# Kernel tuning notes

Measured on AMD Instinct MI355X. Metric: run time of the kernel, lower is better.

The kernel has to match this reference:

```python
import jax, jax.numpy as jnp
import numpy as np
from jax import lax


def _conv3x3(x, w, groups=1):
    # x: [B,C,H,W], w: [O, C//groups, 3, 3], padding=1, no bias
    return lax.conv_general_dilated(
        x, w, window_strides=(1, 1), padding=((1, 1), (1, 1)),
        dimension_numbers=('NCHW', 'OIHW', 'NCHW'),
        feature_group_count=groups)


def _nonlocal_attention(x):
    # q = k = v = flattened features; attn is [B, N, N] with N = H*W
    B, C, H, W = x.shape
    f = x.reshape(B, C, H * W)                                   # [B,C,N]
    attn = jax.nn.softmax(jnp.einsum('bcn,bcm->bnm', f, f), -1)  # [B,N,N]
    out = jnp.einsum('bnm,bcm->bcn', attn, f)                    # [B,C,N]
    return out.reshape(B, C, H, W)


def setup_inputs() -> dict:
    key = jax.random.key(0)
    k1, k2 = jax.random.split(key)
    C = 64
    x = jax.random.normal(k1, (8, C, 64, 64), dtype=jnp.float32)
    # kaiming_normal fan_out for 3x3 conv: std = sqrt(2 / (C*9))
    W_std = jax.random.normal(k2, (C, C, 3, 3), dtype=jnp.float32) * np.float32(np.sqrt(2.0 / (C * 9)))
    return {'x': x, 'W_std': W_std}


def reference(x, W_std):
    B, C, H, W = x.shape
    # FusionDiffConv: standard 3x3 conv + fixed depthwise Laplacian conv
    lap = jnp.array([[0., 1., 0.], [1., -4., 1.], [0., 1., 0.]], dtype=x.dtype)
    W_lap = jnp.broadcast_to(lap[None, None], (C, 1, 3, 3))
    feat = _conv3x3(x, W_std) + _conv3x3(x, W_lap, groups=C)
    # AttentionModule: 3-scale pooled non-local attention pyramid, bilinear upsample, sum
    out = jnp.zeros_like(feat)
    for scale in (4, 2, 1):
        h, w = H // scale, W // scale
        blk = feat.reshape(B, C, h, scale, w, scale).mean(axis=(3, 5))  # adaptive_avg_pool2d (exact divisor)
        blk = _nonlocal_attention(blk)
        # bilinear, half-pixel centers == torch align_corners=False
        out = out + jax.image.resize(blk, (B, C, H, W), method='bilinear')
    return x + out
```

## Files before the change

kernel.cpp:

```cpp
#include <hip/hip_runtime.h>
#include <hip/hip_bf16.h>
#include <math.h>

#define BB 8
#define CC 64
#define HH 64
#define WW 64
#define NPIX (HH*WW)
#define LOG2E 1.44269504088896340736f

typedef __attribute__((ext_vector_type(8))) short bf16x8;
typedef __attribute__((ext_vector_type(8))) _Float16 half8;
typedef __attribute__((ext_vector_type(4))) _Float16 half4;
typedef __attribute__((ext_vector_type(4))) float floatx4;
typedef __attribute__((ext_vector_type(8))) unsigned short ushort8;

__device__ inline unsigned short f2bf(float x) {
  __hip_bfloat16 h = __float2bfloat16(x);
  return *reinterpret_cast<unsigned short*>(&h);
}
__device__ inline unsigned short f2bf_fast(float x) {
  const unsigned u = __float_as_uint(x);
  return (unsigned short)((u + 0x8000u) >> 16);
}
__device__ inline float bf2f(unsigned short u) {
  __hip_bfloat16 h = *reinterpret_cast<__hip_bfloat16*>(&u);
  return __bfloat162float(h);
}
__device__ inline unsigned short f2h(float x) {
  _Float16 h = (_Float16)x;
  return *reinterpret_cast<unsigned short*>(&h);
}
__device__ inline float h2f(unsigned short u) {
  _Float16 h = *reinterpret_cast<_Float16*>(&u);
  return (float)h;
}

__device__ inline int swzoff(int n, int c) {
  return (((c >> 3) ^ (n & 7)) << 3) | (c & 7);
}
__device__ inline int swzvslot(int key, int c) {
  return ((((key >> 2) ^ (c & 15)) << 2)) | (key & 3);
}

#define GLD_LDS16(gp, lp)                                                     \
  __builtin_amdgcn_global_load_lds(                                           \
      (const __attribute__((address_space(1))) void*)(gp),                    \
      (__attribute__((address_space(3))) void*)(lp), 16, 0, 0)

__global__ __launch_bounds__(256) void prep_kernel(
    const float* __restrict__ xin, const float* __restrict__ w,
    unsigned short* __restrict__ xth, unsigned short* __restrict__ xtl,
    unsigned short* __restrict__ wth, unsigned short* __restrict__ wtl) {
  __shared__ float XL[64][65];
  const int bid = blockIdx.x;
  const int tid = threadIdx.x;
  if (bid < 512) {
    const int y = bid & 63, b = bid >> 6;
    const int xq = tid & 15, cw = tid >> 4;
    const float* xb = xin + (size_t)b * CC * NPIX + y * WW;
#pragma unroll
    for (int p = 0; p < 4; ++p) {
      const int c = p * 16 + cw;
      const float4 v = *(const float4*)(xb + (size_t)c * NPIX + xq * 4);
      XL[c][xq * 4 + 0] = v.x; XL[c][xq * 4 + 1] = v.y;
      XL[c][xq * 4 + 2] = v.z; XL[c][xq * 4 + 3] = v.w;
    }
    __syncthreads();
    const int px = tid & 63, cp = tid >> 6;
    const size_t nb = ((size_t)b * NPIX + y * WW + px) * CC;
    ushort8 vh[2], vl[2];
#pragma unroll
    for (int j = 0; j < 16; ++j) {
      const float v = XL[cp * 16 + j][px];
      const unsigned short hh = f2bf(v);
      vh[j >> 3][j & 7] = hh;
      vl[j >> 3][j & 7] = f2bf(v - bf2f(hh));
    }
#pragma unroll
    for (int k = 0; k < 2; ++k) {
      const int ch = cp * 2 + k;
      const int off = ((ch ^ (px & 7)) << 3);
      *(ushort8*)(xth + nb + off) = vh[k];
      *(ushort8*)(xtl + nb + off) = vl[k];
    }
  } else {
    const int idx = (bid - 512) * 256 + tid;
    const int c   = idx & 63;
    const int o   = (idx >> 6) & 63;
    const int tap = idx >> 12;
    float v = w[((o * 64 + c) * 9) + tap];
    if (o == c) {
      const float lapk[9] = {0.f, 1.f, 0.f, 1.f, -4.f, 1.f, 0.f, 1.f, 0.f};
      v += lapk[tap];
    }
    const unsigned short hi = f2bf(v);
    wth[(tap * 64 + o) * 64 + c] = hi;
    wtl[(tap * 64 + o) * 64 + c] = f2bf(v - bf2f(hi));
  }
}

__global__ __launch_bounds__(256, 2) void conv_mfma(
    const unsigned short* __restrict__ xth,
    const unsigned short* __restrict__ xtl,
    const unsigned short* __restrict__ wth,
    const unsigned short* __restrict__ wtl,
    unsigned short* __restrict__ fh, unsigned short* __restrict__ fl,
    unsigned short* __restrict__ fv) {
  __shared__ __align__(16) unsigned short XS[6 * 4096];

  const int tid  = threadIdx.x;
  const int lane = tid & 63;
  const int wave = tid >> 6;
  const int r16  = lane & 15;
  const int quad = lane >> 4;
  const int y = blockIdx.x, b = blockIdx.y;

#pragma unroll
  for (int r = 0; r < 3; ++r) {
    const int yy = min(max(y - 1 + r, 0), HH - 1);
    const unsigned short* sh = xth + ((size_t)b * NPIX + yy * WW) * CC;
    const unsigned short* sl = xtl + ((size_t)b * NPIX + yy * WW) * CC;
    GLD_LDS16(sh + tid * 8,        &XS[r * 4096 + tid * 8]);
    GLD_LDS16(sh + 2048 + tid * 8, &XS[r * 4096 + 2048 + tid * 8]);
    GLD_LDS16(sl + tid * 8,        &XS[(3 + r) * 4096 + tid * 8]);
    GLD_LDS16(sl + 2048 + tid * 8, &XS[(3 + r) * 4096 + 2048 + tid * 8]);
  }
  __syncthreads();

  floatx4 acc[4];
#pragma unroll
  for (int t = 0; t < 4; ++t) acc[t] = (floatx4){0.f, 0.f, 0.f, 0.f};
  const bf16x8 ZF = {0, 0, 0, 0, 0, 0, 0, 0};
  const int og = wave * 16 + r16;

#pragma unroll
  for (int tap = 0; tap < 9; ++tap) {
    const int ky = tap / 3, kx = tap % 3;
    const int yy = y + ky - 1;
    if (yy < 0 || yy >= HH) continue;
    const unsigned short* wt = wth + ((tap * 64 + og) << 6);
    const unsigned short* wl = wtl + ((tap * 64 + og) << 6);
    const bf16x8 Wh0 = *(const bf16x8*)(wt + quad * 8);
    const bf16x8 Wh1 = *(const bf16x8*)(wt + 32 + quad * 8);
    const bf16x8 Wl0 = *(const bf16x8*)(wl + quad * 8);
    const bf16x8 Wl1 = *(const bf16x8*)(wl + 32 + quad * 8);
#pragma unroll
    for (int t = 0; t < 4; ++t) {
      const int px = t * 16 + r16 + kx - 1;
      const bool ok = (px >= 0) && (px < WW);
      const int pxc = ok ? px : 0;
      const int bh = ky * 4096 + pxc * 64;
      const int bl = bh + 3 * 4096;
      const int o0 = ((quad ^ (pxc & 7)) << 3);
      const int o1 = (((4 + quad) ^ (pxc & 7)) << 3);
      bf16x8 Ah0 = *(const bf16x8*)(XS + bh + o0);
      bf16x8 Ah1 = *(const bf16x8*)(XS + bh + o1);
      bf16x8 Al0 = *(const bf16x8*)(XS + bl + o0);
      bf16x8 Al1 = *(const bf16x8*)(XS + bl + o1);
      if (!ok) { Ah0 = ZF; Ah1 = ZF; Al0 = ZF; Al1 = ZF; }
      acc[t] = __builtin_amdgcn_mfma_f32_16x16x32_bf16(Ah0, Wh0, acc[t], 0, 0, 0);
      acc[t] = __builtin_amdgcn_mfma_f32_16x16x32_bf16(Ah1, Wh1, acc[t], 0, 0, 0);
      acc[t] = __builtin_amdgcn_mfma_f32_16x16x32_bf16(Ah0, Wl0, acc[t], 0, 0, 0);
      acc[t] = __builtin_amdgcn_mfma_f32_16x16x32_bf16(Ah1, Wl1, acc[t], 0, 0, 0);
      acc[t] = __builtin_amdgcn_mfma_f32_16x16x32_bf16(Al0, Wh0, acc[t], 0, 0, 0);
      acc[t] = __builtin_amdgcn_mfma_f32_16x16x32_bf16(Al1, Wh1, acc[t], 0, 0, 0);
    }
  }

#pragma unroll
  for (int t = 0; t < 4; ++t)
#pragma unroll
    for (int r = 0; r < 4; ++r) {
      const int key = t * 16 + quad * 4 + r;
      const int n = y * WW + key;
      const float v = acc[t][r];
      const unsigned short hi = f2h(v);
      const unsigned short lo = f2h(v - h2f(hi));
      fh[((size_t)b * NPIX + n) * CC + swzoff(n, og)] = hi;
      fl[((size_t)b * NPIX + n) * CC + swzoff(n, og)] = lo;
      fv[(((size_t)b * (NPIX >> 6) + y) * CC + og) * 64 + swzvslot(key, og)] =
          f2h(v);
    }
}

__global__ void pools_kernel(const unsigned short* __restrict__ in_h,
                             const unsigned short* __restrict__ in_l,
                             unsigned short* __restrict__ h2,
                             unsigned short* __restrict__ l2,
                             unsigned short* __restrict__ v2,
                             unsigned short* __restrict__ h4,
                             unsigned short* __restrict__ l4,
                             unsigned short* __restrict__ v4) {
  const int bid = blockIdx.x;
  if (bid < 2048) {
    const int idx = bid * 256 + threadIdx.x;
    const int c  = idx & 63;
    const int t  = idx >> 6;
    const int xo = t & 31;
    const int yo = (t >> 5) & 31;
    const int b  = t >> 10;
    const size_t ibase = (size_t)b * NPIX * CC;
    float s = 0.f;
#pragma unroll
    for (int dy = 0; dy < 2; ++dy)
#pragma unroll
      for (int dx = 0; dx < 2; ++dx) {
        const int nin = (2*yo+dy) * 64 + (2*xo+dx);
        const size_t a = ibase + (size_t)nin * CC + swzoff(nin, c);
        s += h2f(in_h[a]) + h2f(in_l[a]);
      }
    const float vv = 0.25f * s;
    const unsigned short hi = f2h(vv);
    const int nout = yo * 32 + xo;
    const size_t ob = ((size_t)b * 1024 + nout) * CC + swzoff(nout, c);
    h2[ob] = hi;
    l2[ob] = f2h(vv - h2f(hi));
    v2[(((size_t)b * 16 + (nout >> 6)) * CC + c) * 64 + swzvslot(nout & 63, c)] =
        f2h(vv);
  } else {
    const int idx = (bid - 2048) * 256 + threadIdx.x;
    const int c  = idx & 63;
    const int t  = idx >> 6;
    const int xo = t & 15;
    const int yo = (t >> 4) & 15;
    const int b  = t >> 8;
    const size_t ibase = (size_t)b * NPIX * CC;
    float s = 0.f;
#pragma unroll
    for (int dy = 0; dy < 4; ++dy)
#pragma unroll
      for (int dx = 0; dx < 4; ++dx) {
        const int nin = (4*yo+dy) * 64 + (4*xo+dx);
        const size_t a = ibase + (size_t)nin * CC + swzoff(nin, c);
        s += h2f(in_h[a]) + h2f(in_l[a]);
      }
    const float vv = 0.0625f * s;
    const unsigned short hi = f2h(vv);
    const int nout = yo * 16 + xo;
    const size_t ob = ((size_t)b * 256 + nout) * CC + swzoff(nout, c);
    h4[ob] = hi;
    l4[ob] = f2h(vv - h2f(hi));
    v4[(((size_t)b * 4 + (nout >> 6)) * CC + c) * 64 + swzvslot(nout & 63, c)] =
        f2h(vv);
  }
}

template <int NH, int KS>
__device__ __forceinline__ void attn_body(
    int bid,
    const unsigned short* __restrict__ fh,
    const unsigned short* __restrict__ fl,
    const unsigned short* __restrict__ fv,
    float* __restrict__ outF, unsigned short* __restrict__ outB,
    float* __restrict__ outL, int N,
    unsigned short* KVT) {
  const int tid  = threadIdx.x;
  const int lane = tid & 63;
  const int wave = tid >> 6;
  const int b    = bid & 7;
  const int rest = bid >> 3;
  const int nq   = N / (64 * NH);
  const int qt   = rest % nq;
  const int ks   = rest / nq;
  const int q0   = qt * (64 * NH) + wave * (16 * NH);
  const int nt   = (N >> 6) / KS;
  const int t0   = ks * nt;
  const int r16  = lane & 15;
  const int quad = lane >> 4;
  const int swb  = r16 & 7;

  const unsigned short* fhB = fh + (size_t)b * N * CC;
  const unsigned short* flB = fl + (size_t)b * N * CC;
  const unsigned short* fvB = fv + (size_t)b * N * CC;

  {
    const size_t tb = (size_t)t0 * 4096;
#pragma unroll
    for (int j = 0; j < 4; ++j) {
      const int cid = wave * 4 + j;
      const int arr = cid >> 3, sub = (cid & 7) << 9;
      const unsigned short* g = (arr == 0 ? fhB : fvB) + tb + sub + lane * 8;
      GLD_LDS16(g, KVT + arr * 4096 + sub + lane * 8);
    }
  }

  half8 Qh[NH][2], Ql[NH][2];
  float Mq[NH];
#pragma unroll
  for (int h = 0; h < NH; ++h) {
    float Mpart = 0.f;
#pragma unroll
    for (int kss = 0; kss < 2; ++kss) {
      const size_t off = (size_t)(q0 + h * 16 + r16) * CC
                         + ((((kss << 2) + quad) ^ swb) << 3);
      const ushort8 hh = *(const ushort8*)(fhB + off);
      const ushort8 ll = *(const ushort8*)(flB + off);
      half8 sh, sl;
#pragma unroll
      for (int j = 0; j < 8; ++j) {
        const float f = h2f(hh[j]) + h2f(ll[j]);
        const float g = f * LOG2E;
        const _Float16 gh = (_Float16)g;
        sh[j] = gh;
        sl[j] = (_Float16)(g - (float)gh);
        Mpart += g * f;
      }
      Qh[h][kss] = sh;
      Ql[h][kss] = sl;
    }
    Mpart += __shfl_xor(Mpart, 16, 64);
    Mpart += __shfl_xor(Mpart, 32, 64);
    Mq[h] = Mpart;
  }

  floatx4 O[NH][4];
  float lloc[NH];
#pragma unroll
  for (int h = 0; h < NH; ++h) {
    lloc[h] = 0.f;
#pragma unroll
    for (int ch = 0; ch < 4; ++ch) O[h][ch] = (floatx4){0.f, 0.f, 0.f, 0.f};
  }

  int koff[2];
#pragma unroll
  for (int kss = 0; kss < 2; ++kss) koff[kss] = (((kss << 2) + quad) ^ swb) << 3;

  for (int t = 0; t < nt; ++t) {
    const int cur = t & 1;
    __syncthreads();
    if (t + 1 < nt) {
      const size_t tb = (size_t)(t0 + t + 1) * 4096;
      unsigned short* dst = KVT + (cur ^ 1) * 8192;
#pragma unroll
      for (int j = 0; j < 4; ++j) {
        const int cid = wave * 4 + j;
        const int arr = cid >> 3, sub = (cid & 7) << 9;
        const unsigned short* g = (arr == 0 ? fhB : fvB) + tb + sub + lane * 8;
        GLD_LDS16(g, dst + arr * 4096 + sub + lane * 8);
      }
    }
    const unsigned short* kh = KVT + cur * 8192;
    const unsigned short* vt = kh + 4096;

#pragma unroll
    for (int tt = 0; tt < 4; ++tt) {
      const int kbase = (tt * 16 + r16) * 64;
      const half8 Kh0 = *(const half8*)(kh + kbase + koff[0]);
      const half8 Kh1 = *(const half8*)(kh + kbase + koff[1]);
      const int vslot = (((tt * 4 + quad) ^ r16) << 2);
      half4 Vf[4];
#pragma unroll
      for (int ch = 0; ch < 4; ++ch)
        Vf[ch] = *(const half4*)(vt + (ch * 16 + r16) * 64 + vslot);
#pragma unroll
      for (int h = 0; h < NH; ++h) {
        floatx4 s = (floatx4){0.f, 0.f, 0.f, 0.f};
        s = __builtin_amdgcn_mfma_f32_16x16x32_f16(Kh0, Qh[h][0], s, 0, 0, 0);
        s = __builtin_amdgcn_mfma_f32_16x16x32_f16(Kh1, Qh[h][1], s, 0, 0, 0);
        s = __builtin_amdgcn_mfma_f32_16x16x32_f16(Kh0, Ql[h][0], s, 0, 0, 0);
        s = __builtin_amdgcn_mfma_f32_16x16x32_f16(Kh1, Ql[h][1], s, 0, 0, 0);
        const float p0 = __builtin_amdgcn_exp2f(s[0] - Mq[h]);
        const float p1 = __builtin_amdgcn_exp2f(s[1] - Mq[h]);
        const float p2 = __builtin_amdgcn_exp2f(s[2] - Mq[h]);
        const float p3 = __builtin_amdgcn_exp2f(s[3] - Mq[h]);
        lloc[h] += (p0 + p1) + (p2 + p3);
        const half4 Pf = {(_Float16)p0, (_Float16)p1, (_Float16)p2, (_Float16)p3};
#pragma unroll
        for (int ch = 0; ch < 4; ++ch)
          O[h][ch] = __builtin_amdgcn_mfma_f32_16x16x16f16(Pf, Vf[ch],
                                                           O[h][ch], 0, 0, 0);
      }
    }
  }

#pragma unroll
  for (int h = 0; h < NH; ++h) {
    float lt = lloc[h];
    lt += __shfl_xor(lt, 16, 64);
    lt += __shfl_xor(lt, 32, 64);
    float lq[4];
#pragma unroll
    for (int r = 0; r < 4; ++r) lq[r] = __shfl(lt, quad * 4 + r, 16);
    if (KS != 1 && r16 == 0) {
#pragma unroll
      for (int r = 0; r < 4; ++r)
        outL[(size_t)ks * BB * N + (size_t)b * N + q0 + h * 16 + quad * 4 + r] =
            lq[r];
    }
#pragma unroll
    for (int ch = 0; ch < 4; ++ch)
#pragma unroll
      for (int r = 0; r < 4; ++r) {
        const size_t qi = (size_t)b * N + q0 + h * 16 + quad * 4 + r;
        if (KS == 1) {
          outF[qi * CC + ch * 16 + r16] = O[h][ch][r] / lq[r];
        } else {
          outB[(size_t)ks * BB * N * CC + qi * CC + ch * 16 + r16] =
              f2bf_fast(O[h][ch][r]);
        }
      }
  }
}

__global__ __launch_bounds__(256, 4) void attn_all(
    const unsigned short* __restrict__ fh1, const unsigned short* __restrict__ fl1,
    const unsigned short* __restrict__ fv1,
    unsigned short* __restrict__ Op1, float* __restrict__ Lp1,
    const unsigned short* __restrict__ fh2, const unsigned short* __restrict__ fl2,
    const unsigned short* __restrict__ fv2,
    unsigned short* __restrict__ Op2, float* __restrict__ Lp2,
    const unsigned short* __restrict__ fh4, const unsigned short* __restrict__ fl4,
    const unsigned short* __restrict__ fv4, float* __restrict__ a4) {
  __shared__ __align__(16) unsigned short KVT[2][2 * 4096];
  const int bid = blockIdx.x;
  if (bid < 1024) {
    attn_body<2, 4>(bid, fh1, fl1, fv1, nullptr, Op1, Lp1, NPIX, &KVT[0][0]);
  } else if (bid < 1280) {
    attn_body<1, 2>(bid - 1024, fh2, fl2, fv2, nullptr, Op2, Lp2, 1024,
                    &KVT[0][0]);
  } else {
    attn_body<1, 1>(bid - 1280, fh4, fl4, fv4, a4, nullptr, nullptr, 256,
                    &KVT[0][0]);
  }
}

__global__ __launch_bounds__(256) void final3_kernel(
    const float* __restrict__ xin,
    const unsigned short* __restrict__ Op1, const float* __restrict__ Lp1,
    const unsigned short* __restrict__ Op2, const float* __restrict__ Lp2,
    const float* __restrict__ a4, float* __restrict__ out) {
  __shared__ float T[64][65];
  __shared__ float T2[64][66];
  const int tid = threadIdx.x;
  const int y = blockIdx.x & 63;
  const int b = blockIdx.x >> 6;
  const size_t S1 = (size_t)BB * NPIX * CC;
  const size_t T1 = (size_t)BB * NPIX;
  const size_t S2 = (size_t)BB * 1024 * CC;
  const size_t L2 = (size_t)BB * 1024;

  const float ty2 = y * 0.5f - 0.25f;
  const int iy2 = (int)floorf(ty2);
  const float wy2 = ty2 - iy2;
  const int iy20 = max(iy2, 0), iy21 = min(iy2 + 1, 31);

  const int nl = tid >> 2;
  const int ck = (tid & 3) * 16;

  {
    const int n = y * 64 + nl;
    float lv = 0.f;
#pragma unroll
    for (int ks = 0; ks < 4; ++ks)
      lv += Lp1[(size_t)ks * T1 + (size_t)b * NPIX + n];
    const float inv = 1.f / lv;
    float v[16];
#pragma unroll
    for (int j = 0; j < 16; ++j) v[j] = 0.f;
#pragma unroll
    for (int ks = 0; ks < 4; ++ks) {
      const unsigned short* src =
          Op1 + (size_t)ks * S1 + ((size_t)b * NPIX + n) * CC + ck;
      const ushort8 u0 = *(const ushort8*)(src);
      const ushort8 u1 = *(const ushort8*)(src + 8);
#pragma unroll
      for (int j = 0; j < 8; ++j) {
        v[j]     += bf2f(u0[j]);
        v[8 + j] += bf2f(u1[j]);
      }
    }
#pragma unroll
    for (int j = 0; j < 16; ++j) T[ck + j][nl] = v[j] * inv;
  }
  {
    const int row = nl >> 5;
    const int ix  = nl & 31;
    const int n2  = (row == 0 ? iy20 : iy21) * 32 + ix;
    float lv = Lp2[(size_t)b * 1024 + n2] + Lp2[L2 + (size_t)b * 1024 + n2];
    const float inv = 1.f / lv;
    float v[16];
#pragma unroll
    for (int j = 0; j < 16; ++j) v[j] = 0.f;
#pragma unroll
    for (int ks = 0; ks < 2; ++ks) {
      const unsigned short* src =
          Op2 + (size_t)ks * S2 + ((size_t)b * 1024 + n2) * CC + ck;
      const ushort8 u0 = *(const ushort8*)(src);
      const ushort8 u1 = *(const ushort8*)(src + 8);
#pragma unroll
      for (int j = 0; j < 8; ++j) {
        v[j]     += bf2f(u0[j]);
        v[8 + j] += bf2f(u1[j]);
      }
    }
#pragma unroll
    for (int j = 0; j < 16; ++j) T2[ck + j][nl] = v[j] * inv;
  }
  __syncthreads();

  const int c  = tid >> 2;
  const int xk = (tid & 3) * 16;
  const float* xrow = xin + (((size_t)b * CC + c) * HH + y) * WW;
  float* orow = out + (((size_t)b * CC + c) * HH + y) * WW;

  const float ty4 = y * 0.25f - 0.375f;
  const int iy4 = (int)floorf(ty4);
  const float wy4 = ty4 - iy4;
  const int iy40 = max(iy4, 0), iy41 = min(iy4 + 1, 15);
  const float* b4 = a4 + (size_t)b * 256 * 64 + c;

#pragma unroll
  for (int j = 0; j < 16; ++j) {
    const int xx = xk + j;
    float r = xrow[xx] + T[c][xx];
    {
      const float tx = xx * 0.5f - 0.25f;
      const int ix = (int)floorf(tx);
      const float wx = tx - ix;
      const int ix0 = max(ix, 0), ix1 = min(ix + 1, 31);
      const float v00 = T2[c][ix0],      v01 = T2[c][ix1];
      const float v10 = T2[c][32 + ix0], v11 = T2[c][32 + ix1];
      r += (1.f-wy2)*((1.f-wx)*v00 + wx*v01) + wy2*((1.f-wx)*v10 + wx*v11);
    }
    {
      const float tx = xx * 0.25f - 0.375f;
      const int ix = (int)floorf(tx);
      const float wx = tx - ix;
      const int ix0 = max(ix, 0), ix1 = min(ix + 1, 15);
      const float v00 = b4[(iy40*16+ix0)*64], v01 = b4[(iy40*16+ix1)*64];
      const float v10 = b4[(iy41*16+ix0)*64], v11 = b4[(iy41*16+ix1)*64];
      r += (1.f-wy4)*((1.f-wx)*v00 + wx*v01) + wy4*((1.f-wx)*v10 + wx*v11);
    }
    orow[xx] = r;
  }
}

extern "C" void kernel_launch(void* const* d_in, const int* in_sizes, int n_in,
                              void* d_out, int out_size, void* d_ws,
                              size_t ws_size, hipStream_t stream) {
  const float* x = (const float*)d_in[0];
  const float* w = (const float*)d_in[1];
  float* out = (float*)d_out;

  unsigned short* fh1 = (unsigned short*)d_ws;
  unsigned short* fl1 = fh1 + (size_t)BB*NPIX*CC;
  unsigned short* fv1 = fl1 + (size_t)BB*NPIX*CC;
  unsigned short* fh2 = fv1 + (size_t)BB*NPIX*CC;
  unsigned short* fl2 = fh2 + (size_t)BB*1024*CC;
  unsigned short* fv2 = fl2 + (size_t)BB*1024*CC;
  unsigned short* fh4 = fv2 + (size_t)BB*1024*CC;
  unsigned short* fl4 = fh4 + (size_t)BB*256*CC;
  unsigned short* fv4 = fl4 + (size_t)BB*256*CC;
  unsigned short* Op1 = fv4 + (size_t)BB*256*CC;
  float* Lp1 = (float*)(Op1 + 4*(size_t)BB*NPIX*CC);
  unsigned short* Op2 = (unsigned short*)(Lp1 + 4*(size_t)BB*NPIX);
  float* Lp2 = (float*)(Op2 + 2*(size_t)BB*1024*CC);
  float* a4  = Lp2 + 2*(size_t)BB*1024;

  unsigned short* xth = (unsigned short*)Op1;
  unsigned short* xtl = xth + (size_t)BB*NPIX*CC;
  unsigned short* wth = (unsigned short*)Op2;
  unsigned short* wtl = wth + 9*64*64;

  prep_kernel<<<656, 256, 0, stream>>>(x, w, xth, xtl, wth, wtl);
  conv_mfma<<<dim3(64, 8), 256, 0, stream>>>(xth, xtl, wth, wtl, fh1, fl1, fv1);
  pools_kernel<<<2560, 256, 0, stream>>>(fh1, fl1, fh2, fl2, fv2, fh4, fl4, fv4);
  attn_all<<<1312, 256, 0, stream>>>(fh1, fl1, fv1, Op1, Lp1,
                                     fh2, fl2, fv2, Op2, Lp2,
                                     fh4, fl4, fv4, a4);
  final3_kernel<<<512, 256, 0, stream>>>(x, Op1, Lp1, Op2, Lp2, a4, out);
}
```

Baseline: 154.5 us.

## Fuse input bf16 split into conv kernel and drop Q low-part MFMAs

The separate prep pass that transposed x to NHWC and split it into bf16 hi/lo planes is removed. The conv kernel now loads fp32 rows straight into LDS, converts them and writes the swizzled hi/lo tiles itself, which avoids a full write and re-read of the split input. In attention, the low-order fp16 part of Q is dropped, halving the QK^T MFMAs per tile at the cost of score precision. Each conv block now re-converts three input rows, so the conversion work is repeated about threefold, and it adds extra barriers.

```diff
diff --git a/kernel.cpp b/kernel.cpp
--- a/kernel.cpp
+++ b/kernel.cpp
@@ -48,66 +48,31 @@
       (const __attribute__((address_space(1))) void*)(gp),                    \
       (__attribute__((address_space(3))) void*)(lp), 16, 0, 0)
 
-__global__ __launch_bounds__(256) void prep_kernel(
-    const float* __restrict__ xin, const float* __restrict__ w,
-    unsigned short* __restrict__ xth, unsigned short* __restrict__ xtl,
+__global__ __launch_bounds__(256) void wprep_kernel(
+    const float* __restrict__ w,
     unsigned short* __restrict__ wth, unsigned short* __restrict__ wtl) {
-  __shared__ float XL[64][65];
-  const int bid = blockIdx.x;
-  const int tid = threadIdx.x;
-  if (bid < 512) {
-    const int y = bid & 63, b = bid >> 6;
-    const int xq = tid & 15, cw = tid >> 4;
-    const float* xb = xin + (size_t)b * CC * NPIX + y * WW;
-#pragma unroll
-    for (int p = 0; p < 4; ++p) {
-      const int c = p * 16 + cw;
-      const float4 v = *(const float4*)(xb + (size_t)c * NPIX + xq * 4);
-      XL[c][xq * 4 + 0] = v.x; XL[c][xq * 4 + 1] = v.y;
-      XL[c][xq * 4 + 2] = v.z; XL[c][xq * 4 + 3] = v.w;
-    }
-    __syncthreads();
-    const int px = tid & 63, cp = tid >> 6;
-    const size_t nb = ((size_t)b * NPIX + y * WW + px) * CC;
-    ushort8 vh[2], vl[2];
-#pragma unroll
-    for (int j = 0; j < 16; ++j) {
-      const float v = XL[cp * 16 + j][px];
-      const unsigned short hh = f2bf(v);
-      vh[j >> 3][j & 7] = hh;
-      vl[j >> 3][j & 7] = f2bf(v - bf2f(hh));
-    }
-#pragma unroll
-    for (int k = 0; k < 2; ++k) {
-      const int ch = cp * 2 + k;
-      const int off = ((ch ^ (px & 7)) << 3);
-      *(ushort8*)(xth + nb + off) = vh[k];
-      *(ushort8*)(xtl + nb + off) = vl[k];
-    }
-  } else {
-    const int idx = (bid - 512) * 256 + tid;
-    const int c   = idx & 63;
-    const int o   = (idx >> 6) & 63;
-    const int tap = idx >> 12;
-    float v = w[((o * 64 + c) * 9) + tap];
-    if (o == c) {
-      const float lapk[9] = {0.f, 1.f, 0.f, 1.f, -4.f, 1.f, 0.f, 1.f, 0.f};
-      v += lapk[tap];
-    }
-    const unsigned short hi = f2bf(v);
-    wth[(tap * 64 + o) * 64 + c] = hi;
-    wtl[(tap * 64 + o) * 64 + c] = f2bf(v - bf2f(hi));
-  }
+  const int idx = blockIdx.x * 256 + threadIdx.x;
+  const int c   = idx & 63;
+  const int o   = (idx >> 6) & 63;
+  const int tap = idx >> 12;
+  float v = w[((o * 64 + c) * 9) + tap];
+  if (o == c) {
+    const float lapk[9] = {0.f, 1.f, 0.f, 1.f, -4.f, 1.f, 0.f, 1.f, 0.f};
+    v += lapk[tap];
+  }
+  const unsigned short hi = f2bf(v);
+  wth[(tap * 64 + o) * 64 + c] = hi;
+  wtl[(tap * 64 + o) * 64 + c] = f2bf(v - bf2f(hi));
 }
 
 __global__ __launch_bounds__(256, 2) void conv_mfma(
-    const unsigned short* __restrict__ xth,
-    const unsigned short* __restrict__ xtl,
+    const float* __restrict__ xin,
     const unsigned short* __restrict__ wth,
     const unsigned short* __restrict__ wtl,
     unsigned short* __restrict__ fh, unsigned short* __restrict__ fl,
     unsigned short* __restrict__ fv) {
   __shared__ __align__(16) unsigned short XS[6 * 4096];
+  __shared__ __align__(16) float XLf[64 * 64];
 
   const int tid  = threadIdx.x;
   const int lane = tid & 63;
@@ -115,18 +80,40 @@
   const int r16  = lane & 15;
   const int quad = lane >> 4;
   const int y = blockIdx.x, b = blockIdx.y;
-
+  const int px = tid & 63, cp = tid >> 6;
+
+  const float* xb = xin + (size_t)b * CC * NPIX;
 #pragma unroll
   for (int r = 0; r < 3; ++r) {
     const int yy = min(max(y - 1 + r, 0), HH - 1);
-    const unsigned short* sh = xth + ((size_t)b * NPIX + yy * WW) * CC;
-    const unsigned short* sl = xtl + ((size_t)b * NPIX + yy * WW) * CC;
-    GLD_LDS16(sh + tid * 8,        &XS[r * 4096 + tid * 8]);
-    GLD_LDS16(sh + 2048 + tid * 8, &XS[r * 4096 + 2048 + tid * 8]);
-    GLD_LDS16(sl + tid * 8,        &XS[(3 + r) * 4096 + tid * 8]);
-    GLD_LDS16(sl + 2048 + tid * 8, &XS[(3 + r) * 4096 + 2048 + tid * 8]);
-  }
-  __syncthreads();
+    const float* xrow = xb + yy * WW;
+#pragma unroll
+    for (int j = 0; j < 4; ++j) {
+      const int cb = (wave * 4 + j) * 4;
+      const int cl = cb + (lane >> 4);
+      const float* g = xrow + (size_t)cl * NPIX + ((lane & 15) << 2);
+      GLD_LDS16(g, (char*)XLf + cb * 256 + lane * 16);
+    }
+    __syncthreads();
+    ushort8 vh[2], vl[2];
+#pragma unroll
+    for (int j = 0; j < 16; ++j) {
+      const float v = XLf[(cp * 16 + j) * 64 + px];
+      const unsigned short hh = f2bf(v);
+      vh[j >> 3][j & 7] = hh;
+      vl[j >> 3][j & 7] = f2bf(v - bf2f(hh));
+    }
+    unsigned short* xsh = XS + r * 4096 + px * 64;
+    unsigned short* xsl = XS + (3 + r) * 4096 + px * 64;
+#pragma unroll
+    for (int k = 0; k < 2; ++k) {
+      const int ch = cp * 2 + k;
+      const int off = ((ch ^ (px & 7)) << 3);
+      *(ushort8*)(xsh + off) = vh[k];
+      *(ushort8*)(xsl + off) = vl[k];
+    }
+    __syncthreads();
+  }
 
   floatx4 acc[4];
 #pragma unroll
@@ -147,9 +134,9 @@
     const bf16x8 Wl1 = *(const bf16x8*)(wl + 32 + quad * 8);
 #pragma unroll
     for (int t = 0; t < 4; ++t) {
-      const int px = t * 16 + r16 + kx - 1;
-      const bool ok = (px >= 0) && (px < WW);
-      const int pxc = ok ? px : 0;
+      const int px2 = t * 16 + r16 + kx - 1;
+      const bool ok = (px2 >= 0) && (px2 < WW);
+      const int pxc = ok ? px2 : 0;
       const int bh = ky * 4096 + pxc * 64;
       const int bl = bh + 3 * 4096;
       const int o0 = ((quad ^ (pxc & 7)) << 3);
@@ -285,7 +272,7 @@
     }
   }
 
-  half8 Qh[NH][2], Ql[NH][2];
+  half8 Qh[NH][2];
   float Mq[NH];
 #pragma unroll
   for (int h = 0; h < NH; ++h) {
@@ -296,18 +283,15 @@
                          + ((((kss << 2) + quad) ^ swb) << 3);
       const ushort8 hh = *(const ushort8*)(fhB + off);
       const ushort8 ll = *(const ushort8*)(flB + off);
-      half8 sh, sl;
+      half8 sh;
 #pragma unroll
       for (int j = 0; j < 8; ++j) {
         const float f = h2f(hh[j]) + h2f(ll[j]);
         const float g = f * LOG2E;
-        const _Float16 gh = (_Float16)g;
-        sh[j] = gh;
-        sl[j] = (_Float16)(g - (float)gh);
+        sh[j] = (_Float16)g;
         Mpart += g * f;
       }
       Qh[h][kss] = sh;
-      Ql[h][kss] = sl;
     }
     Mpart += __shfl_xor(Mpart, 16, 64);
     Mpart += __shfl_xor(Mpart, 32, 64);
@@ -359,8 +343,6 @@
         floatx4 s = (floatx4){0.f, 0.f, 0.f, 0.f};
         s = __builtin_amdgcn_mfma_f32_16x16x32_f16(Kh0, Qh[h][0], s, 0, 0, 0);
         s = __builtin_amdgcn_mfma_f32_16x16x32_f16(Kh1, Qh[h][1], s, 0, 0, 0);
-        s = __builtin_amdgcn_mfma_f32_16x16x32_f16(Kh0, Ql[h][0], s, 0, 0, 0);
-        s = __builtin_amdgcn_mfma_f32_16x16x32_f16(Kh1, Ql[h][1], s, 0, 0, 0);
         const float p0 = __builtin_amdgcn_exp2f(s[0] - Mq[h]);
         const float p1 = __builtin_amdgcn_exp2f(s[1] - Mq[h]);
         const float p2 = __builtin_amdgcn_exp2f(s[2] - Mq[h]);
@@ -559,13 +541,11 @@
   float* Lp2 = (float*)(Op2 + 2*(size_t)BB*1024*CC);
   float* a4  = Lp2 + 2*(size_t)BB*1024;
 
-  unsigned short* xth = (unsigned short*)Op1;
-  unsigned short* xtl = xth + (size_t)BB*NPIX*CC;
   unsigned short* wth = (unsigned short*)Op2;
   unsigned short* wtl = wth + 9*64*64;
 
-  prep_kernel<<<656, 256, 0, stream>>>(x, w, xth, xtl, wth, wtl);
-  conv_mfma<<<dim3(64, 8), 256, 0, stream>>>(xth, xtl, wth, wtl, fh1, fl1, fv1);
+  wprep_kernel<<<144, 256, 0, stream>>>(w, wth, wtl);
+  conv_mfma<<<dim3(64, 8), 256, 0, stream>>>(x, wth, wtl, fh1, fl1, fv1);
   pools_kernel<<<2560, 256, 0, stream>>>(fh1, fl1, fh2, fl2, fv2, fh4, fl4, fv4);
   attn_all<<<1312, 256, 0, stream>>>(fh1, fl1, fv1, Op1, Lp1,
                                      fh2, fl2, fv2, Op2, Lp2,
```

After: 144.5 us. 1.07x faster.
